# Performance work log

Hardware: AMD Instinct MI355X
Metric: run time of the kernel (lower is better)

Reference implementation:

```python
import jax, jax.numpy as jnp
import numpy as np

N, DEG, B, DM, NH, DOUT = 100000, 32, 8192, 256, 4, 128
EPS = 1e-6

def rmsnorm(x, w):
    return x * jax.lax.rsqrt(jnp.mean(x * x, axis=-1, keepdims=True) + EPS) * w

def setup_inputs():
    key = jax.random.key(0)
    ks = jax.random.split(key, 16)
    s = 0.02
    H = jax.random.normal(ks[0], (N, DM), jnp.float32)
    # CSR-friendly graph: every node has exactly DEG out-neighbors (src already sorted)
    src = jnp.repeat(jnp.arange(N, dtype=jnp.int32), DEG)
    dst = jax.random.randint(ks[1], (N * DEG,), 0, N, dtype=jnp.int32)
    edge_index = jnp.stack([src, dst])
    centers = jax.random.randint(ks[2], (B,), 0, N, dtype=jnp.int32)
    target = jax.random.normal(ks[3], (N, DOUT), jnp.float32)
    p = lambda k, sh: jax.random.normal(k, sh, jnp.float32) * s
    return dict(
        H=H, edge_index=edge_index, centers=centers, target=target, max_deg=DEG,
        ln_in_w=jnp.ones((DM,), jnp.float32), ln1_w=jnp.ones((DM,), jnp.float32), ln2_w=jnp.ones((DM,), jnp.float32),
        w_qkv=p(ks[4], (3 * DM, DM)), b_qkv=jnp.zeros((3 * DM,), jnp.float32),
        w_o=p(ks[5], (DM, DM)), b_o=jnp.zeros((DM,), jnp.float32),
        w_gate=p(ks[6], (DM, DM)), w_up=p(ks[7], (DM, DM)), w_down=p(ks[8], (DM, DM)),
        w_head=p(ks[9], (DOUT, DM)), b_head=jnp.zeros((DOUT,), jnp.float32),
    )

def _forward(H, target, ln_in_w, ln1_w, ln2_w, w_qkv, b_qkv, w_o, b_o, w_gate, w_up, w_down, w_head, b_head, edge_index, centers, max_deg):
    n, d = H.shape
    Bc = centers.shape[0]
    src, dst = edge_index[0], edge_index[1]
    # CSR-like sort by source (assume_undirected=True: no reverse edges added)
    order = jnp.argsort(src)
    dst_s = dst[order]
    counts = jnp.bincount(src, length=n)
    row_ptr = jnp.concatenate([jnp.zeros((1,), counts.dtype), jnp.cumsum(counts)])
    starts = row_ptr[centers]
    deg = jnp.minimum(row_ptr[centers + 1] - starts, max_deg)  # cap at max_neighbors
    pos = jnp.arange(max_deg)[None, :]
    mask = pos < deg[:, None]                                   # [B, max_deg]
    idx_in = jnp.clip(starts[:, None] + pos, 0, dst_s.shape[0] - 1)
    nbrs = jnp.where(mask, dst_s[idx_in], -1)                   # padded neighbor ids
    idx_mat = jnp.concatenate([centers[:, None].astype(nbrs.dtype), nbrs], axis=1)  # [B, L]
    kpm = idx_mat == -1                                         # key padding mask
    X = H[jnp.maximum(idx_mat, 0)]                              # [B, L, d] star pack
    X = rmsnorm(X, ln_in_w)
    X = jnp.where(kpm[..., None], 0.0, X)
    # encoder block (num_layers = 1): RMSNorm -> MHA -> residual -> RMSNorm -> gated MLP -> residual
    xn = rmsnorm(X, ln1_w)
    qkv = xn @ w_qkv.T + b_qkv
    q, k, v = jnp.split(qkv, 3, axis=-1)
    hd = d // NH
    L = 1 + max_deg
    sh = lambda t: t.reshape(Bc, L, NH, hd).transpose(0, 2, 1, 3)
    qh, kh, vh = sh(q), sh(k), sh(v)
    scores = jnp.einsum('bhqc,bhkc->bhqk', qh, kh) * np.float32(1.0 / np.sqrt(hd))
    scores = jnp.where(kpm[:, None, None, :], -jnp.inf, scores)
    attn = jax.nn.softmax(scores, axis=-1)
    ao = jnp.einsum('bhqk,bhkc->bhqc', attn, vh).transpose(0, 2, 1, 3).reshape(Bc, L, d)
    X = X + ao @ w_o.T + b_o
    xn2 = rmsnorm(X, ln2_w)
    Z = X + (jax.nn.silu(xn2 @ w_gate.T) * (xn2 @ w_up.T)) @ w_down.T
    # per-pair MTP loss on frontier (neighbor) positions, mean_per_center reduction
    y_hat = Z[:, 1:] @ w_head.T + b_head                        # [B, max_deg, DOUT]
    y_true = target[jnp.maximum(nbrs, 0)]
    err = jnp.mean((y_hat - y_true) ** 2, axis=-1)
    err = jnp.where(mask, err, 0.0)
    cnt = jnp.maximum(deg.astype(err.dtype), 1.0)
    return jnp.mean(jnp.sum(err, axis=1) / cnt)

def reference(H, edge_index, centers, target, max_deg, ln_in_w, ln1_w, ln2_w, w_qkv, b_qkv, w_o, b_o, w_gate, w_up, w_down, w_head, b_head):
    return _forward(H, target, ln_in_w, ln1_w, ln2_w, w_qkv, b_qkv, w_o, b_o, w_gate, w_up, w_down, w_head, b_head, edge_index, centers, max_deg)
```

## Files before the change

kernel.cpp:

```cpp
#include <hip/hip_runtime.h>

#define DM 256
#define NH 4
#define HD 64
#define DEG 32
#define LQ 33
#define DOUT 128
#define NTHREADS 256
#define XS 268
#define QS 72

typedef __attribute__((ext_vector_type(8))) short bf8v;
typedef __attribute__((ext_vector_type(4))) float f4v;

__device__ __forceinline__ float b2f(unsigned short u){ union{unsigned int i;float f;}v; v.i=((unsigned int)u)<<16; return v.f; }
__device__ __forceinline__ unsigned short f2b(float f){
  union{float f;unsigned int i;}v; v.f=f;
  unsigned int r=v.i+0x7FFFu+((v.i>>16)&1u);
  return (unsigned short)(r>>16);
}
__device__ __forceinline__ float wred(float x){
  #pragma unroll
  for (int o=32;o>=1;o>>=1) x += __shfl_xor(x,o,64);
  return x;
}

__device__ __forceinline__ int swz(int r, int c){ return r*DM + (((c>>3) ^ (r&7))<<3) + (c&7); }
__device__ __forceinline__ int swzV(int r, int c){ return r*HD + (((c>>3) ^ (r&7))<<3) + (c&7); }

template<bool BF>
__device__ __forceinline__ bf8v wfrag(const float* Wf, const unsigned short* Wb, int row, int e){
  if constexpr (BF) {
    return *(const bf8v*)(Wb + (size_t)row*DM + e);
  } else {
    const float* p = Wf + (size_t)row*DM + e;
    const float4 a = *(const float4*)p;
    const float4 b = *(const float4*)(p+4);
    bf8v r;
    r[0]=(short)(__float_as_uint(a.x)>>16); r[1]=(short)(__float_as_uint(a.y)>>16);
    r[2]=(short)(__float_as_uint(a.z)>>16); r[3]=(short)(__float_as_uint(a.w)>>16);
    r[4]=(short)(__float_as_uint(b.x)>>16); r[5]=(short)(__float_as_uint(b.y)>>16);
    r[6]=(short)(__float_as_uint(b.z)>>16); r[7]=(short)(__float_as_uint(b.w)>>16);
    return r;
  }
}

__device__ __forceinline__ f4v mfma16(bf8v a, bf8v b, f4v c){
  return __builtin_amdgcn_mfma_f32_16x16x32_bf16(a, b, c, 0, 0, 0);
}

#define U_Q  0
#define U_K  3456
#define U_VT 6912
#define U_P  0
#define U_AO 3456
#define U_SZ 12288

template<bool WBF16>
__global__ __launch_bounds__(NTHREADS, 2) void smtp_center(
    const float* __restrict__ H,
    const int* __restrict__ dstE,
    const int* __restrict__ centers,
    const float* __restrict__ target,
    const float* __restrict__ ln_in_w,
    const float* __restrict__ ln1_w,
    const float* __restrict__ ln2_w,
    const float* __restrict__ w_qkv,
    const float* __restrict__ b_qkv,
    const float* __restrict__ w_o,
    const float* __restrict__ b_o,
    const float* __restrict__ w_gate,
    const float* __restrict__ w_up,
    const float* __restrict__ w_down,
    const float* __restrict__ w_head,
    const float* __restrict__ b_head,
    const unsigned short* __restrict__ wb,
    float* __restrict__ partial)
{
  __shared__ __align__(16) unsigned short sX[48*XS];
  __shared__ __align__(16) unsigned short sN[48*DM];
  __shared__ __align__(16) unsigned short U[U_SZ];
  __shared__ int sIdx[48];
  __shared__ float sRed[4];

  const unsigned short* wbQKV = wb;
  const unsigned short* wbO   = wb + 196608;
  const unsigned short* wbG   = wb + 262144;
  const unsigned short* wbU   = wb + 327680;
  const unsigned short* wbD   = wb + 393216;
  const unsigned short* wbH   = wb + 458752;

  const int tid  = threadIdx.x;
  const int lane = tid & 63;
  const int wave = tid >> 6;
  const int bid  = blockIdx.x;
  const int l15  = lane & 15;
  const int l16  = (lane >> 4) * 8;
  const int rsub = (lane >> 4) * 4;

  if (tid < LQ) {
    int ctr = centers[bid];
    sIdx[tid] = (tid == 0) ? ctr : dstE[(size_t)ctr*DEG + (tid-1)];
  }
  __syncthreads();

  for (int r = wave; r < LQ; r += 4) {
    const float4 x4 = ((const float4*)(H + (size_t)sIdx[r]*DM))[lane];
    float ss = x4.x*x4.x + x4.y*x4.y + x4.z*x4.z + x4.w*x4.w;
    ss = wred(ss);
    const float rs = rsqrtf(ss*(1.f/DM) + 1e-6f);
    const float4 wi = ((const float4*)ln_in_w)[lane];
    const float xv0 = x4.x*rs*wi.x, xv1 = x4.y*rs*wi.y, xv2 = x4.z*rs*wi.z, xv3 = x4.w*rs*wi.w;
    ushort4 xb; xb.x=f2b(xv0); xb.y=f2b(xv1); xb.z=f2b(xv2); xb.w=f2b(xv3);
    ((ushort4*)(sX + r*XS))[lane] = xb;
    float s2 = xv0*xv0 + xv1*xv1 + xv2*xv2 + xv3*xv3;
    s2 = wred(s2);
    const float rs2 = rsqrtf(s2*(1.f/DM) + 1e-6f);
    const float4 w1 = ((const float4*)ln1_w)[lane];
    ushort4 yb; yb.x=f2b(xv0*rs2*w1.x); yb.y=f2b(xv1*rs2*w1.y); yb.z=f2b(xv2*rs2*w1.z); yb.w=f2b(xv3*rs2*w1.w);
    *(ushort4*)(sN + swz(r, lane*4)) = yb;
  }
  {
    ushort4 z4; z4.x=0; z4.y=0; z4.z=0; z4.w=0;
    for (int r = LQ + wave; r < 48; r += 4) {
      ((ushort4*)(sX + r*XS))[lane] = z4;
      ((ushort4*)(sN + r*DM))[lane] = z4;
    }
    if (tid < 128) {
      const int d = tid >> 1, ch = 6 + (tid & 1);
      *(uint4*)&U[U_VT + d*HD + ((ch ^ (d&7))<<3)] = make_uint4(0,0,0,0);
    }
  }
  __syncthreads();

  for (int h = 0; h < NH; ++h) {
    for (int t3 = 0; t3 < 3; ++t3) {
      const int t = wave*3 + t3;
      const int col = t*16 + l15;
      const int sect = t >> 2;
      const int c = col & 63;
      const int wrow = sect*DM + h*HD + c;
      const float bias = b_qkv[wrow];
      f4v acc[3];
      acc[0] = (f4v){bias,bias,bias,bias}; acc[1] = acc[0]; acc[2] = acc[0];
      #pragma unroll
      for (int k = 0; k < 8; ++k) {
        const bf8v b = wfrag<WBF16>(w_qkv, wbQKV, wrow, k*32 + l16);
        #pragma unroll
        for (int m = 0; m < 3; ++m) {
          const bf8v a = *(const bf8v*)(sN + swz(m*16 + l15, k*32 + l16));
          acc[m] = mfma16(a, b, acc[m]);
        }
      }
      if (sect == 2) {
        #pragma unroll
        for (int m = 0; m < 3; ++m)
          #pragma unroll
          for (int j = 0; j < 4; ++j)
            U[U_VT + swzV(c, m*16 + rsub + j)] = f2b(acc[m][j]);
      } else {
        unsigned short* dstb = U + (sect ? U_K : U_Q);
        #pragma unroll
        for (int m = 0; m < 3; ++m)
          #pragma unroll
          for (int j = 0; j < 4; ++j)
            dstb[(m*16 + rsub + j)*QS + c] = f2b(acc[m][j]);
      }
    }
    __syncthreads();

    f4v s3[3];
    s3[0] = (f4v){0.f,0.f,0.f,0.f}; s3[1] = s3[0]; s3[2] = s3[0];
    if (wave < 3) {
      #pragma unroll
      for (int kk = 0; kk < 2; ++kk) {
        const bf8v a = *(const bf8v*)(U + U_Q + (wave*16 + l15)*QS + kk*32 + l16);
        #pragma unroll
        for (int nk = 0; nk < 3; ++nk) {
          const bf8v bb = *(const bf8v*)(U + U_K + (nk*16 + l15)*QS + kk*32 + l16);
          s3[nk] = mfma16(a, bb, s3[nk]);
        }
      }
    }
    __syncthreads();

    if (wave == 3) {
      for (int i = lane; i < 96; i += 64) {
        const int r = i >> 1, ch = 6 + (i & 1);
        *(uint4*)&U[U_P + r*HD + ((ch ^ (r&7))<<3)] = make_uint4(0,0,0,0);
      }
    } else {
      #pragma unroll
      for (int j = 0; j < 4; ++j) {
        const float v0 = s3[0][j]*0.125f;
        const float v1 = s3[1][j]*0.125f;
        const float v2 = (l15 >= 1) ? -INFINITY : s3[2][j]*0.125f;
        float mx = fmaxf(fmaxf(v0, v1), v2);
        mx = fmaxf(mx, __shfl_xor(mx, 1, 64));
        mx = fmaxf(mx, __shfl_xor(mx, 2, 64));
        mx = fmaxf(mx, __shfl_xor(mx, 4, 64));
        mx = fmaxf(mx, __shfl_xor(mx, 8, 64));
        const float e0 = __expf(v0 - mx), e1 = __expf(v1 - mx), e2 = __expf(v2 - mx);
        float den = e0 + e1 + e2;
        den += __shfl_xor(den, 1, 64);
        den += __shfl_xor(den, 2, 64);
        den += __shfl_xor(den, 4, 64);
        den += __shfl_xor(den, 8, 64);
        const float rn = 1.f / den;
        const int row = wave*16 + rsub + j;
        U[U_P + swzV(row, 0*16 + l15)] = f2b(e0 * rn);
        U[U_P + swzV(row, 1*16 + l15)] = f2b(e1 * rn);
        U[U_P + swzV(row, 2*16 + l15)] = f2b(e2 * rn);
      }
    }
    __syncthreads();

    {
      f4v o4[3];
      o4[0] = (f4v){0.f,0.f,0.f,0.f}; o4[1] = o4[0]; o4[2] = o4[0];
      #pragma unroll
      for (int kk = 0; kk < 2; ++kk) {
        const bf8v bb = *(const bf8v*)(U + U_VT + swzV(wave*16 + l15, kk*32 + l16));
        #pragma unroll
        for (int mq = 0; mq < 3; ++mq) {
          const bf8v a = *(const bf8v*)(U + U_P + swzV(mq*16 + l15, kk*32 + l16));
          o4[mq] = mfma16(a, bb, o4[mq]);
        }
      }
      #pragma unroll
      for (int mq = 0; mq < 3; ++mq)
        #pragma unroll
        for (int j = 0; j < 4; ++j)
          U[U_AO + swzV(mq*16 + rsub + j, wave*16 + l15)] = f2b(o4[mq][j]);
    }
    __syncthreads();

    for (int t4 = 0; t4 < 4; ++t4) {
      const int col = (wave*4 + t4)*16 + l15;
      const float bo = (h==0) ? b_o[col] : 0.f;
      f4v acc[3];
      #pragma unroll
      for (int m = 0; m < 3; ++m) {
        #pragma unroll
        for (int j = 0; j < 4; ++j)
          acc[m][j] = b2f(sX[(m*16 + rsub + j)*XS + col]) + bo;
      }
      #pragma unroll
      for (int k = 0; k < 2; ++k) {
        const bf8v b = wfrag<WBF16>(w_o, wbO, col, h*HD + k*32 + l16);
        #pragma unroll
        for (int m = 0; m < 3; ++m) {
          const bf8v a = *(const bf8v*)(U + U_AO + swzV(m*16 + l15, k*32 + l16));
          acc[m] = mfma16(a, b, acc[m]);
        }
      }
      #pragma unroll
      for (int m = 0; m < 3; ++m)
        #pragma unroll
        for (int j = 0; j < 4; ++j)
          sX[(m*16 + rsub + j)*XS + col] = f2b(acc[m][j]);
    }
    __syncthreads();
  }

  for (int r = wave; r < LQ; r += 4) {
    const ushort4 xb = ((const ushort4*)(sX + r*XS))[lane];
    const float x0 = b2f(xb.x), x1 = b2f(xb.y), x2 = b2f(xb.z), x3 = b2f(xb.w);
    float ss = x0*x0 + x1*x1 + x2*x2 + x3*x3;
    ss = wred(ss);
    const float rs = rsqrtf(ss*(1.f/DM) + 1e-6f);
    const float4 w2 = ((const float4*)ln2_w)[lane];
    ushort4 yb; yb.x=f2b(x0*rs*w2.x); yb.y=f2b(x1*rs*w2.y); yb.z=f2b(x2*rs*w2.z); yb.w=f2b(x3*rs*w2.w);
    *(ushort4*)(sN + swz(r, lane*4)) = yb;
  }
  __syncthreads();

  for (int t4 = 0; t4 < 4; ++t4) {
    const int col = (wave*4 + t4)*16 + l15;
    f4v aG[3], aU[3];
    #pragma unroll
    for (int m = 0; m < 3; ++m) { aG[m] = (f4v){0.f,0.f,0.f,0.f}; aU[m] = aG[m]; }
    #pragma unroll
    for (int k = 0; k < 8; ++k) {
      const bf8v bg = wfrag<WBF16>(w_gate, wbG, col, k*32 + l16);
      const bf8v bu = wfrag<WBF16>(w_up,   wbU, col, k*32 + l16);
      #pragma unroll
      for (int m = 0; m < 3; ++m) {
        const bf8v a = *(const bf8v*)(sN + swz(m*16 + l15, k*32 + l16));
        aG[m] = mfma16(a, bg, aG[m]);
        aU[m] = mfma16(a, bu, aU[m]);
      }
    }
    #pragma unroll
    for (int m = 0; m < 3; ++m)
      #pragma unroll
      for (int j = 0; j < 4; ++j) {
        const float g = aG[m][j];
        const float v = (g / (1.f + __expf(-g))) * aU[m][j];
        U[swz(m*16 + rsub + j, col)] = f2b(v);
      }
  }
  __syncthreads();

  for (int t4 = 0; t4 < 4; ++t4) {
    const int col = (wave*4 + t4)*16 + l15;
    f4v acc[3];
    #pragma unroll
    for (int m = 0; m < 3; ++m) {
      #pragma unroll
      for (int j = 0; j < 4; ++j)
        acc[m][j] = b2f(sX[(m*16 + rsub + j)*XS + col]);
    }
    #pragma unroll
    for (int k = 0; k < 8; ++k) {
      const bf8v b = wfrag<WBF16>(w_down, wbD, col, k*32 + l16);
      #pragma unroll
      for (int m = 0; m < 3; ++m) {
        const bf8v a = *(const bf8v*)(U + swz(m*16 + l15, k*32 + l16));
        acc[m] = mfma16(a, b, acc[m]);
      }
    }
    #pragma unroll
    for (int m = 0; m < 3; ++m)
      #pragma unroll
      for (int j = 0; j < 4; ++j)
        sN[swz(m*16 + rsub + j, col)] = f2b(acc[m][j]);
  }
  __syncthreads();

  float lsum = 0.f;
  for (int t2 = 0; t2 < 2; ++t2) {
    const int col = (wave*2 + t2)*16 + l15;
    const float bh = b_head[col];
    f4v acc[2];
    acc[0] = (f4v){bh,bh,bh,bh}; acc[1] = acc[0];
    #pragma unroll
    for (int k = 0; k < 8; ++k) {
      const bf8v b = wfrag<WBF16>(w_head, wbH, col, k*32 + l16);
      #pragma unroll
      for (int m = 0; m < 2; ++m) {
        const bf8v a = *(const bf8v*)(sN + swz(1 + m*16 + l15, k*32 + l16));
        acc[m] = mfma16(a, b, acc[m]);
      }
    }
    #pragma unroll
    for (int m = 0; m < 2; ++m)
      #pragma unroll
      for (int j = 0; j < 4; ++j) {
        const int row = 1 + m*16 + rsub + j;
        const float tv = target[(size_t)sIdx[row]*DOUT + col];
        const float d = acc[m][j] - tv;
        lsum += d*d;
      }
  }
  lsum = wred(lsum);
  if (lane == 0) sRed[wave] = lsum;
  __syncthreads();
  if (tid == 0)
    partial[bid] = (sRed[0]+sRed[1]+sRed[2]+sRed[3]) * (1.f/(DEG*DOUT));
}

__global__ void cvt_w(const float* __restrict__ qkv, const float* __restrict__ o,
                      const float* __restrict__ g, const float* __restrict__ u,
                      const float* __restrict__ dn, const float* __restrict__ hd,
                      unsigned short* __restrict__ out)
{
  const int i = blockIdx.x*NTHREADS + threadIdx.x;
  const int e = i*2;
  if (e >= 491520) return;
  const float* src; int off;
  if      (e < 196608){ src=qkv; off=e; }
  else if (e < 262144){ src=o;  off=e-196608; }
  else if (e < 327680){ src=g;  off=e-262144; }
  else if (e < 393216){ src=u;  off=e-327680; }
  else if (e < 458752){ src=dn; off=e-393216; }
  else                { src=hd; off=e-458752; }
  const float2 v = *(const float2*)(src + off);
  const unsigned int pk = (unsigned int)f2b(v.x) | ((unsigned int)f2b(v.y) << 16);
  *(unsigned int*)(out + e) = pk;
}

__global__ void smtp_reduce(const float* __restrict__ partial, int B, float* __restrict__ out)
{
  __shared__ float sRed[4];
  const int tid = threadIdx.x;
  float s = 0.f;
  for (int i = tid; i < B; i += NTHREADS) s += partial[i];
  s = wred(s);
  if ((tid & 63) == 0) sRed[tid>>6] = s;
  __syncthreads();
  if (tid == 0) out[0] = (sRed[0]+sRed[1]+sRed[2]+sRed[3]) / (float)B;
}

extern "C" void kernel_launch(void* const* d_in, const int* in_sizes, int n_in,
                              void* d_out, int out_size, void* d_ws, size_t ws_size,
                              hipStream_t stream) {
  const float* H        = (const float*)d_in[0];
  const int*   edge     = (const int*)d_in[1];
  const int*   centers  = (const int*)d_in[2];
  const float* target   = (const float*)d_in[3];
  const float* ln_in_w  = (const float*)d_in[5];
  const float* ln1_w    = (const float*)d_in[6];
  const float* ln2_w    = (const float*)d_in[7];
  const float* w_qkv    = (const float*)d_in[8];
  const float* b_qkv    = (const float*)d_in[9];
  const float* w_o      = (const float*)d_in[10];
  const float* b_o      = (const float*)d_in[11];
  const float* w_gate   = (const float*)d_in[12];
  const float* w_up     = (const float*)d_in[13];
  const float* w_down   = (const float*)d_in[14];
  const float* w_head   = (const float*)d_in[15];
  const float* b_head   = (const float*)d_in[16];

  const int B = in_sizes[2];
  const int E = in_sizes[1] / 2;
  const int* dstE = edge + E;

  const size_t WB_ELEMS = 491520;
  const size_t NEED = WB_ELEMS*2 + (size_t)B*4;
  const bool useBf = (ws_size >= NEED);

  if (useBf) {
    unsigned short* wb = (unsigned short*)d_ws;
    float* partial = (float*)((char*)d_ws + WB_ELEMS*2);
    cvt_w<<<960, NTHREADS, 0, stream>>>(w_qkv, w_o, w_gate, w_up, w_down, w_head, wb);
    smtp_center<true><<<B, NTHREADS, 0, stream>>>(H, dstE, centers, target, ln_in_w, ln1_w, ln2_w,
        w_qkv, b_qkv, w_o, b_o, w_gate, w_up, w_down, w_head, b_head, wb, partial);
    smtp_reduce<<<1, NTHREADS, 0, stream>>>(partial, B, (float*)d_out);
  } else {
    float* partial = (float*)d_ws;
    smtp_center<false><<<B, NTHREADS, 0, stream>>>(H, dstE, centers, target, ln_in_w, ln1_w, ln2_w,
        w_qkv, b_qkv, w_o, b_o, w_gate, w_up, w_down, w_head, b_head, (const unsigned short*)d_ws, partial);
    smtp_reduce<<<1, NTHREADS, 0, stream>>>(partial, B, (float*)d_out);
  }
}
```

Before: 1.219 ms.

## Keep residual stream in registers, drop sX LDS buffer, raise occupancy

Moves the residual X from a bf16 LDS buffer into fp32 MFMA accumulator registers (regX) held across all heads, the O-projection and the down-projection. RMSnorm2 now uses cross-wave partial sums kept in a small LDS array. It also compacts the U scratch layout by reusing the Q region for the probabilities, folds the P zeroing into the QK step, drops one barrier per head, and raises launch bounds to 3 blocks per CU. The aim is lower LDS use, fewer barriers and higher occupancy. In exchange it carries 48 extra fp32 registers per thread, which may spill under the tighter register budget.

After: 2.546 ms. +108.8%, slower.

```diff
diff --git a/kernel.cpp b/kernel.cpp
--- a/kernel.cpp
+++ b/kernel.cpp
@@ -7,8 +7,6 @@
 #define LQ 33
 #define DOUT 128
 #define NTHREADS 256
-#define XS 268
-#define QS 72
 
 typedef __attribute__((ext_vector_type(8))) short bf8v;
 typedef __attribute__((ext_vector_type(4))) float f4v;
@@ -50,14 +48,13 @@
 }
 
 #define U_Q  0
-#define U_K  3456
-#define U_VT 6912
-#define U_P  0
-#define U_AO 3456
-#define U_SZ 12288
+#define U_K  3072
+#define U_VT 6144
+#define U_AO 10240
+#define U_SZ 13312
 
 template<bool WBF16>
-__global__ __launch_bounds__(NTHREADS, 2) void smtp_center(
+__global__ __launch_bounds__(NTHREADS, 3) void smtp_center(
     const float* __restrict__ H,
     const int* __restrict__ dstE,
     const int* __restrict__ centers,
@@ -77,9 +74,9 @@
     const unsigned short* __restrict__ wb,
     float* __restrict__ partial)
 {
-  __shared__ __align__(16) unsigned short sX[48*XS];
   __shared__ __align__(16) unsigned short sN[48*DM];
   __shared__ __align__(16) unsigned short U[U_SZ];
+  __shared__ float sRowSum[48*4];
   __shared__ int sIdx[48];
   __shared__ float sRed[4];
 
@@ -112,7 +109,7 @@
     const float4 wi = ((const float4*)ln_in_w)[lane];
     const float xv0 = x4.x*rs*wi.x, xv1 = x4.y*rs*wi.y, xv2 = x4.z*rs*wi.z, xv3 = x4.w*rs*wi.w;
     ushort4 xb; xb.x=f2b(xv0); xb.y=f2b(xv1); xb.z=f2b(xv2); xb.w=f2b(xv3);
-    ((ushort4*)(sX + r*XS))[lane] = xb;
+    *(ushort4*)(U + swz(r, lane*4)) = xb;
     float s2 = xv0*xv0 + xv1*xv1 + xv2*xv2 + xv3*xv3;
     s2 = wred(s2);
     const float rs2 = rsqrtf(s2*(1.f/DM) + 1e-6f);
@@ -123,17 +120,35 @@
   {
     ushort4 z4; z4.x=0; z4.y=0; z4.z=0; z4.w=0;
     for (int r = LQ + wave; r < 48; r += 4) {
-      ((ushort4*)(sX + r*XS))[lane] = z4;
-      ((ushort4*)(sN + r*DM))[lane] = z4;
-    }
-    if (tid < 128) {
-      const int d = tid >> 1, ch = 6 + (tid & 1);
-      *(uint4*)&U[U_VT + d*HD + ((ch ^ (d&7))<<3)] = make_uint4(0,0,0,0);
-    }
-  }
-  __syncthreads();
+      *(ushort4*)(U  + swz(r, lane*4)) = z4;
+      ((ushort4*)(sN + r*DM))[lane]    = z4;
+    }
+  }
+  __syncthreads();
+
+  f4v regX[3][4];
+  {
+    #pragma unroll
+    for (int t4 = 0; t4 < 4; ++t4) {
+      const int col = wave*64 + t4*16 + l15;
+      const float bo = b_o[col];
+      #pragma unroll
+      for (int m = 0; m < 3; ++m)
+        #pragma unroll
+        for (int j = 0; j < 4; ++j)
+          regX[m][t4][j] = b2f(U[swz(m*16 + rsub + j, col)]) + bo;
+    }
+  }
+  __syncthreads();
+
+  if (tid < 128) {
+    const int d = tid >> 1;
+    const int key = 48 + (tid & 1)*8;
+    *(uint4*)&U[U_VT + swzV(d, key)] = make_uint4(0,0,0,0);
+  }
 
   for (int h = 0; h < NH; ++h) {
+    #pragma unroll
     for (int t3 = 0; t3 < 3; ++t3) {
       const int t = wave*3 + t3;
       const int col = t*16 + l15;
@@ -164,32 +179,23 @@
         for (int m = 0; m < 3; ++m)
           #pragma unroll
           for (int j = 0; j < 4; ++j)
-            dstb[(m*16 + rsub + j)*QS + c] = f2b(acc[m][j]);
+            dstb[swzV(m*16 + rsub + j, c)] = f2b(acc[m][j]);
       }
     }
     __syncthreads();
 
-    f4v s3[3];
-    s3[0] = (f4v){0.f,0.f,0.f,0.f}; s3[1] = s3[0]; s3[2] = s3[0];
     if (wave < 3) {
+      f4v s3[3];
+      s3[0] = (f4v){0.f,0.f,0.f,0.f}; s3[1] = s3[0]; s3[2] = s3[0];
       #pragma unroll
       for (int kk = 0; kk < 2; ++kk) {
-        const bf8v a = *(const bf8v*)(U + U_Q + (wave*16 + l15)*QS + kk*32 + l16);
+        const bf8v a = *(const bf8v*)(U + U_Q + swzV(wave*16 + l15, kk*32 + l16));
         #pragma unroll
         for (int nk = 0; nk < 3; ++nk) {
-          const bf8v bb = *(const bf8v*)(U + U_K + (nk*16 + l15)*QS + kk*32 + l16);
+          const bf8v bb = *(const bf8v*)(U + U_K + swzV(nk*16 + l15, kk*32 + l16));
           s3[nk] = mfma16(a, bb, s3[nk]);
         }
       }
-    }
-    __syncthreads();
-
-    if (wave == 3) {
-      for (int i = lane; i < 96; i += 64) {
-        const int r = i >> 1, ch = 6 + (i & 1);
-        *(uint4*)&U[U_P + r*HD + ((ch ^ (r&7))<<3)] = make_uint4(0,0,0,0);
-      }
-    } else {
       #pragma unroll
       for (int j = 0; j < 4; ++j) {
         const float v0 = s3[0][j]*0.125f;
@@ -208,9 +214,9 @@
         den += __shfl_xor(den, 8, 64);
         const float rn = 1.f / den;
         const int row = wave*16 + rsub + j;
-        U[U_P + swzV(row, 0*16 + l15)] = f2b(e0 * rn);
-        U[U_P + swzV(row, 1*16 + l15)] = f2b(e1 * rn);
-        U[U_P + swzV(row, 2*16 + l15)] = f2b(e2 * rn);
+        U[U_Q + swzV(row, 0*16 + l15)] = f2b(e0 * rn);
+        U[U_Q + swzV(row, 1*16 + l15)] = f2b(e1 * rn);
+        U[U_Q + swzV(row, 2*16 + l15)] = f2b(e2 * rn);
       }
     }
     __syncthreads();
@@ -223,7 +229,7 @@
         const bf8v bb = *(const bf8v*)(U + U_VT + swzV(wave*16 + l15, kk*32 + l16));
         #pragma unroll
         for (int mq = 0; mq < 3; ++mq) {
-          const bf8v a = *(const bf8v*)(U + U_P + swzV(mq*16 + l15, kk*32 + l16));
+          const bf8v a = *(const bf8v*)(U + U_Q + swzV(mq*16 + l15, kk*32 + l16));
           o4[mq] = mfma16(a, bb, o4[mq]);
         }
       }
@@ -235,48 +241,56 @@
     }
     __syncthreads();
 
+    #pragma unroll
     for (int t4 = 0; t4 < 4; ++t4) {
-      const int col = (wave*4 + t4)*16 + l15;
-      const float bo = (h==0) ? b_o[col] : 0.f;
-      f4v acc[3];
-      #pragma unroll
-      for (int m = 0; m < 3; ++m) {
-        #pragma unroll
-        for (int j = 0; j < 4; ++j)
-          acc[m][j] = b2f(sX[(m*16 + rsub + j)*XS + col]) + bo;
-      }
+      const int col = wave*64 + t4*16 + l15;
       #pragma unroll
       for (int k = 0; k < 2; ++k) {
         const bf8v b = wfrag<WBF16>(w_o, wbO, col, h*HD + k*32 + l16);
         #pragma unroll
         for (int m = 0; m < 3; ++m) {
           const bf8v a = *(const bf8v*)(U + U_AO + swzV(m*16 + l15, k*32 + l16));
-          acc[m] = mfma16(a, b, acc[m]);
+          regX[m][t4] = mfma16(a, b, regX[m][t4]);
         }
       }
+    }
+  }
+
+  #pragma unroll
+  for (int m = 0; m < 3; ++m)
+    #pragma unroll
+    for (int j = 0; j < 4; ++j) {
+      float p = 0.f;
+      #pragma unroll
+      for (int t4 = 0; t4 < 4; ++t4) p += regX[m][t4][j]*regX[m][t4][j];
+      p += __shfl_xor(p, 1, 64);
+      p += __shfl_xor(p, 2, 64);
+      p += __shfl_xor(p, 4, 64);
+      p += __shfl_xor(p, 8, 64);
+      if (l15 == 0) sRowSum[(m*16 + rsub + j)*4 + wave] = p;
+    }
+  __syncthreads();
+  {
+    #pragma unroll
+    for (int t4 = 0; t4 < 4; ++t4) {
+      const int col = wave*64 + t4*16 + l15;
+      const float w2 = ln2_w[col];
       #pragma unroll
       for (int m = 0; m < 3; ++m)
         #pragma unroll
-        for (int j = 0; j < 4; ++j)
-          sX[(m*16 + rsub + j)*XS + col] = f2b(acc[m][j]);
-    }
-    __syncthreads();
-  }
-
-  for (int r = wave; r < LQ; r += 4) {
-    const ushort4 xb = ((const ushort4*)(sX + r*XS))[lane];
-    const float x0 = b2f(xb.x), x1 = b2f(xb.y), x2 = b2f(xb.z), x3 = b2f(xb.w);
-    float ss = x0*x0 + x1*x1 + x2*x2 + x3*x3;
-    ss = wred(ss);
-    const float rs = rsqrtf(ss*(1.f/DM) + 1e-6f);
-    const float4 w2 = ((const float4*)ln2_w)[lane];
-    ushort4 yb; yb.x=f2b(x0*rs*w2.x); yb.y=f2b(x1*rs*w2.y); yb.z=f2b(x2*rs*w2.z); yb.w=f2b(x3*rs*w2.w);
-    *(ushort4*)(sN + swz(r, lane*4)) = yb;
-  }
-  __syncthreads();
-
+        for (int j = 0; j < 4; ++j) {
+          const int row = m*16 + rsub + j;
+          const float tot = sRowSum[row*4+0] + sRowSum[row*4+1] + sRowSum[row*4+2] + sRowSum[row*4+3];
+          const float rs = rsqrtf(tot*(1.f/DM) + 1e-6f);
+          sN[swz(row, col)] = f2b(regX[m][t4][j] * rs * w2);
+        }
+    }
+  }
+  __syncthreads();
+
+  #pragma unroll
   for (int t4 = 0; t4 < 4; ++t4) {
-    const int col = (wave*4 + t4)*16 + l15;
+    const int col = wave*64 + t4*16 + l15;
     f4v aG[3], aU[3];
     #pragma unroll
     for (int m = 0; m < 3; ++m) { aG[m] = (f4v){0.f,0.f,0.f,0.f}; aU[m] = aG[m]; }
@@ -302,33 +316,30 @@
   }
   __syncthreads();
 
+  #pragma unroll
   for (int t4 = 0; t4 < 4; ++t4) {
-    const int col = (wave*4 + t4)*16 + l15;
-    f4v acc[3];
-    #pragma unroll
-    for (int m = 0; m < 3; ++m) {
-      #pragma unroll
-      for (int j = 0; j < 4; ++j)
-        acc[m][j] = b2f(sX[(m*16 + rsub + j)*XS + col]);
-    }
+    const int col = wave*64 + t4*16 + l15;
+    f4v acc = regX[0][t4];
+    f4v acc1 = regX[1][t4];
+    f4v acc2 = regX[2][t4];
     #pragma unroll
     for (int k = 0; k < 8; ++k) {
       const bf8v b = wfrag<WBF16>(w_down, wbD, col, k*32 + l16);
-      #pragma unroll
-      for (int m = 0; m < 3; ++m) {
-        const bf8v a = *(const bf8v*)(U + swz(m*16 + l15, k*32 + l16));
-        acc[m] = mfma16(a, b, acc[m]);
-      }
-    }
-    #pragma unroll
-    for (int m = 0; m < 3; ++m)
-      #pragma unroll
-      for (int j = 0; j < 4; ++j)
-        sN[swz(m*16 + rsub + j, col)] = f2b(acc[m][j]);
+      acc  = mfma16(*(const bf8v*)(U + swz(0*16 + l15, k*32 + l16)), b, acc);
+      acc1 = mfma16(*(const bf8v*)(U + swz(1*16 + l15, k*32 + l16)), b, acc1);
+      acc2 = mfma16(*(const bf8v*)(U + swz(2*16 + l15, k*32 + l16)), b, acc2);
+    }
+    #pragma unroll
+    for (int j = 0; j < 4; ++j) {
+      sN[swz(0*16 + rsub + j, col)] = f2b(acc[j]);
+      sN[swz(1*16 + rsub + j, col)] = f2b(acc1[j]);
+      sN[swz(2*16 + rsub + j, col)] = f2b(acc2[j]);
+    }
   }
   __syncthreads();
 
   float lsum = 0.f;
+  #pragma unroll
   for (int t2 = 0; t2 < 2; ++t2) {
     const int col = (wave*2 + t2)*16 + l15;
     const float bh = b_head[col];
```
